# Performance work log

Measured on AMD Instinct MI355X. Metric: run time of the kernel, lower is better.

## Reference

```python
import jax, jax.numpy as jnp
import numpy as np

PLANE_SIZE = 512
N_LEVELS = 8
FEATURE_DIM = 16
N_PTS = 524288


def setup_inputs() -> dict:
    key = jax.random.key(0)
    k1, k2, k3 = jax.random.split(key, 3)
    x = jax.random.uniform(k1, (N_PTS, 3), dtype=jnp.float32)
    # per-point float mip level bias in [0, n_levels-1]
    level = jax.random.uniform(k2, (N_PTS, 1), dtype=jnp.float32) * (N_LEVELS - 1)
    fm = jax.random.uniform(k3, (3, PLANE_SIZE, PLANE_SIZE, FEATURE_DIM),
                            minval=-0.01, maxval=0.01, dtype=jnp.float32)
    return {"x": x, "level": level, "fm": fm, "n_levels": N_LEVELS}


def _bilinear(flat_pyr, offsets, sizes, uv, lvl_i):
    # flat_pyr: (3, T, C) concatenated mip levels; uv: (3, N, 2); lvl_i: (3, N) int32
    size = sizes[lvl_i]                      # (3, N) texture size at this mip
    fsize = size.astype(uv.dtype)
    px = uv[..., 0] * fsize - 0.5            # u -> width axis (nvdiffrast convention)
    py = uv[..., 1] * fsize - 0.5            # v -> height axis
    x0 = jnp.floor(px)
    y0 = jnp.floor(py)
    fx = (px - x0)[..., None]
    fy = (py - y0)[..., None]
    x0i = x0.astype(jnp.int32)
    y0i = y0.astype(jnp.int32)
    xa = jnp.clip(x0i, 0, size - 1)          # boundary_mode='clamp'
    xb = jnp.clip(x0i + 1, 0, size - 1)
    ya = jnp.clip(y0i, 0, size - 1)
    yb = jnp.clip(y0i + 1, 0, size - 1)
    base = offsets[lvl_i]
    p = jnp.arange(3)[:, None]
    g = lambda yy, xx: flat_pyr[p, base + yy * size + xx]   # (3, N, C) gather
    f00 = g(ya, xa); f01 = g(ya, xb); f10 = g(yb, xa); f11 = g(yb, xb)
    return (f00 * (1 - fx) + f01 * fx) * (1 - fy) + (f10 * (1 - fx) + f11 * fx) * fy


def reference(x, level, fm, n_levels):
    N = x.shape[0]
    C = fm.shape[-1]
    # build mip pyramid via 2x2 box filter (nvdiffrast auto-mips)
    levels = [fm]
    for _ in range(n_levels - 1):
        t = levels[-1]
        s = t.shape[1]
        levels.append(t.reshape(3, s // 2, 2, s // 2, 2, C).mean(axis=(2, 4)))
    sizes_list = [l.shape[1] for l in levels]
    offsets = jnp.asarray(np.cumsum([0] + [s * s for s in sizes_list[:-1]]), jnp.int32)
    sizes = jnp.asarray(sizes_list, jnp.int32)
    flat_pyr = jnp.concatenate([l.reshape(3, -1, C) for l in levels], axis=1)  # (3, T, C)
    # tri-plane decomposition: plane0 sees (y,z), plane1 (x,z), plane2 (x,y)
    uv = jnp.stack([x[:, [1, 2]], x[:, [0, 2]], x[:, [0, 1]]], axis=0)  # (3, N, 2)
    max_mip = n_levels - 1
    lvl = jnp.clip(jnp.broadcast_to(level.reshape(1, N), (3, N)), 0.0, float(max_mip))
    l0 = jnp.floor(lvl)
    f = (lvl - l0)[..., None]                # (3, N, 1) level fraction
    l0i = l0.astype(jnp.int32)
    l1i = jnp.minimum(l0i + 1, max_mip)
    s0 = _bilinear(flat_pyr, offsets, sizes, uv, l0i)
    s1 = _bilinear(flat_pyr, offsets, sizes, uv, l1i)
    enc = s0 * (1 - f) + s1 * f              # (3, N, C) trilinear (mip-lerped)
    # permute(1,2,0,3).view(N, 3C): per point, concat plane0|plane1|plane2 features
    return jnp.transpose(enc, (1, 0, 2)).reshape(N, 3 * C)
```

## Files before the change

### kernel.cpp

```cpp
#include <hip/hip_runtime.h>
#include <hip/hip_fp16.h>


typedef float        f4v   __attribute__((ext_vector_type(4)));
typedef unsigned int u32x2 __attribute__((ext_vector_type(2)));
typedef unsigned int u32x4 __attribute__((ext_vector_type(4)));

#define FM_PLANE_STRIDE (262144 * 16)
#define WS_PLANE_STRIDE (87376 * 16)
#define PSTRIDE_H (349520 * 16)
#define WS_H_BYTES (3ull * PSTRIDE_H * 2ull)
#define LVL5_OFF 349184u

__device__ __forceinline__ unsigned lvl_off(int l) {
    return (1048576u - (1048576u >> (2 * l))) / 3u;
}

__device__ __forceinline__ f4v ld4(const float* p) {
    return *reinterpret_cast<const f4v*>(p);
}
__device__ __forceinline__ f4v ld4nt(const float* p) {
    return __builtin_nontemporal_load(reinterpret_cast<const f4v*>(p));
}
__device__ __forceinline__ void st4(float* p, f4v v) {
    *reinterpret_cast<f4v*>(p) = v;
}
__device__ __forceinline__ void st4nt(float* p, f4v v) {
    __builtin_nontemporal_store(v, reinterpret_cast<f4v*>(p));
}
__device__ __forceinline__ f4v ldraw_h(const __half* p) {
    return *reinterpret_cast<const f4v*>(p);
}
__device__ __forceinline__ u32x2 pack4(f4v v) {
    __half2 lo = __floats2half2_rn(v.x, v.y);
    __half2 hi = __floats2half2_rn(v.z, v.w);
    u32x2 r;
    r.x = *reinterpret_cast<unsigned*>(&lo);
    r.y = *reinterpret_cast<unsigned*>(&hi);
    return r;
}
__device__ __forceinline__ f4v h4f(const __half* p) {
    u32x2 u = *reinterpret_cast<const u32x2*>(p);
    unsigned a0 = u.x, a1 = u.y;
    __half2 lo = *reinterpret_cast<__half2*>(&a0);
    __half2 hi = *reinterpret_cast<__half2*>(&a1);
    float2 flo = __half22float2(lo), fhi = __half22float2(hi);
    f4v r; r.x = flo.x; r.y = flo.y; r.z = fhi.x; r.w = fhi.y;
    return r;
}
__device__ __forceinline__ float2 up2(float rawcomp) {
    unsigned u = __float_as_uint(rawcomp);
    __half2 hh = *reinterpret_cast<__half2*>(&u);
    return __half22float2(hh);
}


__global__ __launch_bounds__(256) void mip_convert_l1(
    const float* __restrict__ fm, __half* __restrict__ wsh)
{
    int t = blockIdx.x * 256 + threadIdx.x;
    const int p = blockIdx.y;
    const int q = t & 3, idx = t >> 2;
    const int y = idx >> 8, x = idx & 255;
    const float* sp = fm + (size_t)p * FM_PLANE_STRIDE
                         + ((size_t)(2 * y) * 512 + 2 * x) * 16 + q * 4;
    f4v a = ld4nt(sp);
    f4v b = ld4nt(sp + 16);
    f4v c = ld4nt(sp + 512 * 16);
    f4v d = ld4nt(sp + 512 * 16 + 16);
    __half* L0 = wsh + (size_t)p * PSTRIDE_H;
    size_t o00 = ((size_t)(2 * y) * 512 + 2 * x) * 16 + q * 4;
    *reinterpret_cast<u32x2*>(L0 + o00)                 = pack4(a);
    *reinterpret_cast<u32x2*>(L0 + o00 + 16)            = pack4(b);
    *reinterpret_cast<u32x2*>(L0 + o00 + 512 * 16)      = pack4(c);
    *reinterpret_cast<u32x2*>(L0 + o00 + 512 * 16 + 16) = pack4(d);
    f4v m = (a + b + c + d) * 0.25f;
    __half* L1 = wsh + (size_t)p * PSTRIDE_H + (size_t)262144 * 16;
    *reinterpret_cast<u32x2*>(L1 + ((size_t)y * 256 + x) * 16 + q * 4) = pack4(m);
}

__global__ __launch_bounds__(256) void mip_tail_h(__half* __restrict__ wsh)
{
    const int tile = blockIdx.x;
    const int q    = blockIdx.y;
    const int p    = blockIdx.z;
    const int ty = tile >> 2, tx = tile & 3;
    const int tid = threadIdx.x;

    __shared__ f4v A[32 * 32];
    __shared__ f4v B[16 * 16];

    __half* plane = wsh + (size_t)p * PSTRIDE_H;
    const __half* L1 = plane + (size_t)lvl_off(1) * 16;
    __half* L2 = plane + (size_t)lvl_off(2) * 16;
    __half* L3 = plane + (size_t)lvl_off(3) * 16;
    __half* L4 = plane + (size_t)lvl_off(4) * 16;
    __half* L5 = plane + (size_t)lvl_off(5) * 16;
    __half* L6 = plane + (size_t)lvl_off(6) * 16;
    __half* L7 = plane + (size_t)lvl_off(7) * 16;

    #pragma unroll
    for (int k = 0; k < 4; ++k) {
        int li = tid + k * 256;
        int ly = li >> 5, lx = li & 31;
        int gy = ty * 32 + ly, gx = tx * 32 + lx;
        const __half* sp = L1 + ((size_t)(2 * gy) * 256 + 2 * gx) * 16 + q * 4;
        f4v r = (h4f(sp) + h4f(sp + 16) + h4f(sp + 256 * 16) + h4f(sp + 256 * 16 + 16)) * 0.25f;
        A[li] = r;
        *reinterpret_cast<u32x2*>(L2 + ((size_t)gy * 128 + gx) * 16 + q * 4) = pack4(r);
    }
    __syncthreads();

    {
        int ly = tid >> 4, lx = tid & 15;
        f4v r = (A[(2 * ly) * 32 + 2 * lx]     + A[(2 * ly) * 32 + 2 * lx + 1] +
                 A[(2 * ly + 1) * 32 + 2 * lx] + A[(2 * ly + 1) * 32 + 2 * lx + 1]) * 0.25f;
        B[tid] = r;
        *reinterpret_cast<u32x2*>(L3 + ((size_t)(ty * 16 + ly) * 64 + tx * 16 + lx) * 16 + q * 4) = pack4(r);
    }
    __syncthreads();

    if (tid < 64) {
        int ly = tid >> 3, lx = tid & 7;
        f4v r = (B[(2 * ly) * 16 + 2 * lx]     + B[(2 * ly) * 16 + 2 * lx + 1] +
                 B[(2 * ly + 1) * 16 + 2 * lx] + B[(2 * ly + 1) * 16 + 2 * lx + 1]) * 0.25f;
        A[tid] = r;
        *reinterpret_cast<u32x2*>(L4 + ((size_t)(ty * 8 + ly) * 32 + tx * 8 + lx) * 16 + q * 4) = pack4(r);
    }
    __syncthreads();

    if (tid < 16) {
        int ly = tid >> 2, lx = tid & 3;
        f4v r = (A[(2 * ly) * 8 + 2 * lx]     + A[(2 * ly) * 8 + 2 * lx + 1] +
                 A[(2 * ly + 1) * 8 + 2 * lx] + A[(2 * ly + 1) * 8 + 2 * lx + 1]) * 0.25f;
        B[tid] = r;
        *reinterpret_cast<u32x2*>(L5 + ((size_t)(ty * 4 + ly) * 16 + tx * 4 + lx) * 16 + q * 4) = pack4(r);
    }
    __syncthreads();

    if (tid < 4) {
        int ly = tid >> 1, lx = tid & 1;
        f4v r = (B[(2 * ly) * 4 + 2 * lx]     + B[(2 * ly) * 4 + 2 * lx + 1] +
                 B[(2 * ly + 1) * 4 + 2 * lx] + B[(2 * ly + 1) * 4 + 2 * lx + 1]) * 0.25f;
        A[tid] = r;
        *reinterpret_cast<u32x2*>(L6 + ((size_t)(ty * 2 + ly) * 8 + tx * 2 + lx) * 16 + q * 4) = pack4(r);
    }
    __syncthreads();

    if (tid == 0) {
        f4v r = (A[0] + A[1] + A[2] + A[3]) * 0.25f;
        *reinterpret_cast<u32x2*>(L7 + ((size_t)ty * 4 + tx) * 16 + q * 4) = pack4(r);
    }
}

__device__ __forceinline__ void tap_issue(
    const __half* __restrict__ wsh, const __half* __restrict__ lds_h,
    int p, int l, float u, float v, int h,
    f4v& q00, f4v& q01, f4v& q10, f4v& q11, float& fx, float& fy)
{
    const int sz = 512 >> l;
    const float fsz = (float)sz;
    float px = u * fsz - 0.5f;
    float py = v * fsz - 0.5f;
    float xf = floorf(px), yf = floorf(py);
    fx = px - xf;
    fy = py - yf;
    int xi = (int)xf, yi = (int)yf;
    int xa = min(max(xi, 0), sz - 1);
    int xb = min(xi + 1, sz - 1);
    int ya = min(max(yi, 0), sz - 1);
    int yb = min(yi + 1, sz - 1);
    if (l >= 5) {
        const int sel = (l == 6) ? 256 : ((l == 7) ? 320 : 0);
        const __half* base = lds_h + (size_t)(p * 336 + sel) * 16 + h * 8;
        const __half* r0 = base + (ya * sz) * 16;
        const __half* r1 = base + (yb * sz) * 16;
        q00 = ldraw_h(r0 + xa * 16);
        q01 = ldraw_h(r0 + xb * 16);
        q10 = ldraw_h(r1 + xa * 16);
        q11 = ldraw_h(r1 + xb * 16);
    } else {
        const __half* base = wsh + (size_t)p * PSTRIDE_H + (size_t)lvl_off(l) * 16 + h * 8;
        const __half* r0 = base + (size_t)(ya * sz) * 16;
        const __half* r1 = base + (size_t)(yb * sz) * 16;
        q00 = ldraw_h(r0 + (size_t)xa * 16);
        q01 = ldraw_h(r0 + (size_t)xb * 16);
        q10 = ldraw_h(r1 + (size_t)xa * 16);
        q11 = ldraw_h(r1 + (size_t)xb * 16);
    }
}

__global__ __launch_bounds__(512, 8) void trimip_sample_h(
    const float* __restrict__ xyz, const float* __restrict__ level,
    const __half* __restrict__ wsh, float* __restrict__ out, int N)
{
    __shared__ u32x4 lds[2016];
    for (int uidx = threadIdx.x; uidx < 2016; uidx += 512) {
        int p = uidx / 672;
        int rem = uidx - p * 672;
        lds[uidx] = *reinterpret_cast<const u32x4*>(
            wsh + (size_t)p * PSTRIDE_H + (size_t)LVL5_OFF * 16 + (size_t)rem * 8);
    }
    __syncthreads();
    const __half* lds_h = reinterpret_cast<const __half*>(lds);

    int t = blockIdx.x * 512 + threadIdx.x;
    if (t >= N * 6) return;
    const int h = t & 1;
    const int r = t >> 1;
    const int n = r / 3;
    const int p = r - n * 3;

    const float c0 = xyz[n * 3 + 0];
    const float c1 = xyz[n * 3 + 1];
    const float c2 = xyz[n * 3 + 2];
    const float u = (p == 0) ? c1 : c0;
    const float v = (p == 2) ? c1 : c2;

    float lv = level[n];
    lv = fminf(fmaxf(lv, 0.f), 7.f);
    float lf = floorf(lv);
    float f = lv - lf;
    int l0 = (int)lf;
    int l1 = min(l0 + 1, 7);

    f4v a00, a01, a10, a11, b00, b01, b10, b11;
    float fx0, fy0, fx1, fy1;
    tap_issue(wsh, lds_h, p, l0, u, v, h, a00, a01, a10, a11, fx0, fy0);
    tap_issue(wsh, lds_h, p, l1, u, v, h, b00, b01, b10, b11, fx1, fy1);

    float s0[8], s1[8];
    {
        float gx = 1.f - fx0, gy = 1.f - fy0;
        float w00 = gx * gy, w01 = fx0 * gy, w10 = gx * fy0, w11 = fx0 * fy0;
        #pragma unroll
        for (int i = 0; i < 4; ++i) {
            float2 a = up2(a00[i]), b = up2(a01[i]), c = up2(a10[i]), d = up2(a11[i]);
            s0[2 * i]     = a.x * w00 + b.x * w01 + c.x * w10 + d.x * w11;
            s0[2 * i + 1] = a.y * w00 + b.y * w01 + c.y * w10 + d.y * w11;
        }
    }
    {
        float gx = 1.f - fx1, gy = 1.f - fy1;
        float w00 = gx * gy, w01 = fx1 * gy, w10 = gx * fy1, w11 = fx1 * fy1;
        #pragma unroll
        for (int i = 0; i < 4; ++i) {
            float2 a = up2(b00[i]), b = up2(b01[i]), c = up2(b10[i]), d = up2(b11[i]);
            s1[2 * i]     = a.x * w00 + b.x * w01 + c.x * w10 + d.x * w11;
            s1[2 * i + 1] = a.y * w00 + b.y * w01 + c.y * w10 + d.y * w11;
        }
    }

    float g = 1.f - f;
    f4v oa, ob;
    #pragma unroll
    for (int i = 0; i < 4; ++i) {
        oa[i] = s0[i] * g + s1[i] * f;
        ob[i] = s0[4 + i] * g + s1[4 + i] * f;
    }
    st4nt(out + (size_t)t * 8, oa);
    st4nt(out + (size_t)t * 8 + 4, ob);
}


__device__ __forceinline__ f4v avg4(f4v a, f4v b, f4v c, f4v d) {
    return (a + b + c + d) * 0.25f;
}

__global__ __launch_bounds__(256) void mip_build_f(
    const float* __restrict__ src, float* __restrict__ dst)
{
    int t = blockIdx.x * blockDim.x + threadIdx.x;
    const int p = blockIdx.y;
    const int q = t & 3, idx = t >> 2;
    const int y = idx >> 8, x = idx & 255;
    const float* sp = src + (size_t)p * FM_PLANE_STRIDE
                          + ((size_t)(2 * y) * 512 + 2 * x) * 16 + q * 4;
    f4v r = avg4(ld4(sp), ld4(sp + 16), ld4(sp + 512 * 16), ld4(sp + 512 * 16 + 16));
    st4(dst + (size_t)p * WS_PLANE_STRIDE + ((size_t)y * 256 + x) * 16 + q * 4, r);
}

__global__ __launch_bounds__(256) void mip_tail_f(float* __restrict__ mips)
{
    const int tile = blockIdx.x, q = blockIdx.y, p = blockIdx.z;
    const int ty = tile >> 2, tx = tile & 3;
    const int tid = threadIdx.x;
    __shared__ f4v A[32 * 32];
    __shared__ f4v B[16 * 16];
    float* plane = mips + (size_t)p * WS_PLANE_STRIDE;
    const float* L1 = plane;
    float* L2 = plane + (size_t)65536 * 16;
    float* L3 = plane + (size_t)81920 * 16;
    float* L4 = plane + (size_t)86016 * 16;
    float* L5 = plane + (size_t)87040 * 16;
    float* L6 = plane + (size_t)87296 * 16;
    float* L7 = plane + (size_t)87360 * 16;

    #pragma unroll
    for (int k = 0; k < 4; ++k) {
        int li = tid + k * 256;
        int ly = li >> 5, lx = li & 31;
        int gy = ty * 32 + ly, gx = tx * 32 + lx;
        const float* sp = L1 + ((size_t)(2 * gy) * 256 + 2 * gx) * 16 + q * 4;
        f4v r = avg4(ld4(sp), ld4(sp + 16), ld4(sp + 256 * 16), ld4(sp + 256 * 16 + 16));
        A[li] = r;
        st4(L2 + ((size_t)gy * 128 + gx) * 16 + q * 4, r);
    }
    __syncthreads();
    {
        int ly = tid >> 4, lx = tid & 15;
        f4v r = avg4(A[(2 * ly) * 32 + 2 * lx],     A[(2 * ly) * 32 + 2 * lx + 1],
                     A[(2 * ly + 1) * 32 + 2 * lx], A[(2 * ly + 1) * 32 + 2 * lx + 1]);
        B[tid] = r;
        st4(L3 + ((size_t)(ty * 16 + ly) * 64 + tx * 16 + lx) * 16 + q * 4, r);
    }
    __syncthreads();
    if (tid < 64) {
        int ly = tid >> 3, lx = tid & 7;
        f4v r = avg4(B[(2 * ly) * 16 + 2 * lx],     B[(2 * ly) * 16 + 2 * lx + 1],
                     B[(2 * ly + 1) * 16 + 2 * lx], B[(2 * ly + 1) * 16 + 2 * lx + 1]);
        A[tid] = r;
        st4(L4 + ((size_t)(ty * 8 + ly) * 32 + tx * 8 + lx) * 16 + q * 4, r);
    }
    __syncthreads();
    if (tid < 16) {
        int ly = tid >> 2, lx = tid & 3;
        f4v r = avg4(A[(2 * ly) * 8 + 2 * lx],     A[(2 * ly) * 8 + 2 * lx + 1],
                     A[(2 * ly + 1) * 8 + 2 * lx], A[(2 * ly + 1) * 8 + 2 * lx + 1]);
        B[tid] = r;
        st4(L5 + ((size_t)(ty * 4 + ly) * 16 + tx * 4 + lx) * 16 + q * 4, r);
    }
    __syncthreads();
    if (tid < 4) {
        int ly = tid >> 1, lx = tid & 1;
        f4v r = avg4(B[(2 * ly) * 4 + 2 * lx],     B[(2 * ly) * 4 + 2 * lx + 1],
                     B[(2 * ly + 1) * 4 + 2 * lx], B[(2 * ly + 1) * 4 + 2 * lx + 1]);
        A[tid] = r;
        st4(L6 + ((size_t)(ty * 2 + ly) * 8 + tx * 2 + lx) * 16 + q * 4, r);
    }
    __syncthreads();
    if (tid == 0) {
        f4v r = avg4(A[0], A[1], A[2], A[3]);
        st4(L7 + ((size_t)ty * 4 + tx) * 16 + q * 4, r);
    }
}

__device__ __forceinline__ f4v bilerp_f(
    const float* __restrict__ fm, const float* __restrict__ mips,
    int p, int l, float u, float v, int q)
{
    const int sz = 512 >> l;
    const float fsz = (float)sz;
    float px = u * fsz - 0.5f;
    float py = v * fsz - 0.5f;
    float xf = floorf(px), yf = floorf(py);
    float fx = px - xf, fy = py - yf;
    int xi = (int)xf, yi = (int)yf;
    int xa = min(max(xi, 0), sz - 1);
    int xb = min(xi + 1, sz - 1);
    int ya = min(max(yi, 0), sz - 1);
    int yb = min(yi + 1, sz - 1);
    const float* base;
    if (l == 0) {
        base = fm + (size_t)p * FM_PLANE_STRIDE;
    } else {
        unsigned off = (262144u - ((unsigned)(sz * sz) << 2)) / 3u;
        base = mips + (size_t)p * WS_PLANE_STRIDE + (size_t)off * 16;
    }
    const float* r0 = base + (size_t)(ya * sz) * 16 + q * 4;
    const float* r1 = base + (size_t)(yb * sz) * 16 + q * 4;
    f4v f00 = ld4(r0 + xa * 16);
    f4v f01 = ld4(r0 + xb * 16);
    f4v f10 = ld4(r1 + xa * 16);
    f4v f11 = ld4(r1 + xb * 16);
    float gx = 1.f - fx, gy = 1.f - fy;
    return (f00 * gx + f01 * fx) * gy + (f10 * gx + f11 * fx) * fy;
}

__global__ __launch_bounds__(256) void trimip_sample_f(
    const float* __restrict__ xyz, const float* __restrict__ level,
    const float* __restrict__ fm, const float* __restrict__ mips,
    float* __restrict__ out, int N)
{
    int t = blockIdx.x * blockDim.x + threadIdx.x;
    if (t >= N * 12) return;
    const int q = t & 3;
    const int r = t >> 2;
    const int n = r / 3;
    const int p = r - n * 3;
    const float c0 = xyz[n * 3 + 0];
    const float c1 = xyz[n * 3 + 1];
    const float c2 = xyz[n * 3 + 2];
    const float u = (p == 0) ? c1 : c0;
    const float v = (p == 2) ? c1 : c2;
    float lv = level[n];
    lv = fminf(fmaxf(lv, 0.f), 7.f);
    float lf = floorf(lv);
    float f = lv - lf;
    int l0 = (int)lf;
    int l1 = min(l0 + 1, 7);
    f4v s0 = bilerp_f(fm, mips, p, l0, u, v, q);
    f4v s1 = bilerp_f(fm, mips, p, l1, u, v, q);
    f4v o = s0 * (1.f - f) + s1 * f;
    st4nt(out + (size_t)t * 4, o);
}

extern "C" void kernel_launch(void* const* d_in, const int* in_sizes, int n_in,
                              void* d_out, int out_size, void* d_ws, size_t ws_size,
                              hipStream_t stream) {
    const float* xyz   = (const float*)d_in[0];
    const float* level = (const float*)d_in[1];
    const float* fm    = (const float*)d_in[2];
    float* out = (float*)d_out;
    const int N = in_sizes[1];

    if (ws_size >= WS_H_BYTES) {
        __half* wsh = (__half*)d_ws;
        mip_convert_l1<<<dim3(1024, 3), dim3(256), 0, stream>>>(fm, wsh);
        mip_tail_h<<<dim3(16, 4, 3), dim3(256), 0, stream>>>(wsh);
        const int total = N * 6;
        trimip_sample_h<<<(total + 511) / 512, 512, 0, stream>>>(xyz, level, wsh, out, N);
    } else {
        float* mips = (float*)d_ws;
        mip_build_f<<<dim3(1024, 3), dim3(256), 0, stream>>>(fm, mips);
        mip_tail_f<<<dim3(16, 4, 3), dim3(256), 0, stream>>>(mips);
        const int total = N * 12;
        trimip_sample_f<<<(total + 255) / 256, 256, 0, stream>>>(xyz, level, fm, mips, out, N);
    }
}
```

Baseline: 200.8 us.

## Split sampling grid per plane and stage mip levels 4-7 in LDS

```diff
diff --git a/kernel.cpp b/kernel.cpp
--- a/kernel.cpp
+++ b/kernel.cpp
@@ -10,7 +10,7 @@
 #define WS_PLANE_STRIDE (87376 * 16)
 #define PSTRIDE_H (349520 * 16)
 #define WS_H_BYTES (3ull * PSTRIDE_H * 2ull)
-#define LVL5_OFF 349184u
+#define LVL4_OFF 348160u
 
 __device__ __forceinline__ unsigned lvl_off(int l) {
     return (1048576u - (1048576u >> (2 * l))) / 3u;
@@ -154,8 +154,8 @@
 }
 
 __device__ __forceinline__ void tap_issue(
-    const __half* __restrict__ wsh, const __half* __restrict__ lds_h,
-    int p, int l, float u, float v, int h,
+    const __half* __restrict__ wplane, const __half* __restrict__ lds_h,
+    int l, float u, float v, int h,
     f4v& q00, f4v& q01, f4v& q10, f4v& q11, float& fx, float& fy)
 {
     const int sz = 512 >> l;
@@ -170,9 +170,8 @@
     int xb = min(xi + 1, sz - 1);
     int ya = min(max(yi, 0), sz - 1);
     int yb = min(yi + 1, sz - 1);
-    if (l >= 5) {
-        const int sel = (l == 6) ? 256 : ((l == 7) ? 320 : 0);
-        const __half* base = lds_h + (size_t)(p * 336 + sel) * 16 + h * 8;
+    if (l >= 4) {
+        const __half* base = lds_h + (size_t)(lvl_off(l) - LVL4_OFF) * 16 + h * 8;
         const __half* r0 = base + (ya * sz) * 16;
         const __half* r1 = base + (yb * sz) * 16;
         q00 = ldraw_h(r0 + xa * 16);
@@ -180,7 +179,7 @@
         q10 = ldraw_h(r1 + xa * 16);
         q11 = ldraw_h(r1 + xb * 16);
     } else {
-        const __half* base = wsh + (size_t)p * PSTRIDE_H + (size_t)lvl_off(l) * 16 + h * 8;
+        const __half* base = wplane + (size_t)lvl_off(l) * 16 + h * 8;
         const __half* r0 = base + (size_t)(ya * sz) * 16;
         const __half* r1 = base + (size_t)(yb * sz) * 16;
         q00 = ldraw_h(r0 + (size_t)xa * 16);
@@ -190,26 +189,23 @@
     }
 }
 
-__global__ __launch_bounds__(512, 8) void trimip_sample_h(
+__global__ __launch_bounds__(512) void trimip_sample_h(
     const float* __restrict__ xyz, const float* __restrict__ level,
     const __half* __restrict__ wsh, float* __restrict__ out, int N)
 {
-    __shared__ u32x4 lds[2016];
-    for (int uidx = threadIdx.x; uidx < 2016; uidx += 512) {
-        int p = uidx / 672;
-        int rem = uidx - p * 672;
+    __shared__ u32x4 lds[2720];
+    const int p = blockIdx.y;
+    const __half* wplane = wsh + (size_t)p * PSTRIDE_H;
+    for (int uidx = threadIdx.x; uidx < 2720; uidx += 512) {
         lds[uidx] = *reinterpret_cast<const u32x4*>(
-            wsh + (size_t)p * PSTRIDE_H + (size_t)LVL5_OFF * 16 + (size_t)rem * 8);
+            wplane + (size_t)LVL4_OFF * 16 + (size_t)uidx * 8);
     }
     __syncthreads();
     const __half* lds_h = reinterpret_cast<const __half*>(lds);
 
-    int t = blockIdx.x * 512 + threadIdx.x;
-    if (t >= N * 6) return;
-    const int h = t & 1;
-    const int r = t >> 1;
-    const int n = r / 3;
-    const int p = r - n * 3;
+    const int n = blockIdx.x * 256 + (threadIdx.x >> 1);
+    if (n >= N) return;
+    const int h = threadIdx.x & 1;
 
     const float c0 = xyz[n * 3 + 0];
     const float c1 = xyz[n * 3 + 1];
@@ -226,8 +222,8 @@
 
     f4v a00, a01, a10, a11, b00, b01, b10, b11;
     float fx0, fy0, fx1, fy1;
-    tap_issue(wsh, lds_h, p, l0, u, v, h, a00, a01, a10, a11, fx0, fy0);
-    tap_issue(wsh, lds_h, p, l1, u, v, h, b00, b01, b10, b11, fx1, fy1);
+    tap_issue(wplane, lds_h, l0, u, v, h, a00, a01, a10, a11, fx0, fy0);
+    tap_issue(wplane, lds_h, l1, u, v, h, b00, b01, b10, b11, fx1, fy1);
 
     float s0[8], s1[8];
     {
@@ -258,8 +254,9 @@
         oa[i] = s0[i] * g + s1[i] * f;
         ob[i] = s0[4 + i] * g + s1[4 + i] * f;
     }
-    st4nt(out + (size_t)t * 8, oa);
-    st4nt(out + (size_t)t * 8 + 4, ob);
+    float* op = out + (size_t)((n * 3 + p) * 2 + h) * 8;
+    st4nt(op, oa);
+    st4nt(op + 4, ob);
 }
 
 
@@ -418,8 +415,8 @@
         __half* wsh = (__half*)d_ws;
         mip_convert_l1<<<dim3(1024, 3), dim3(256), 0, stream>>>(fm, wsh);
         mip_tail_h<<<dim3(16, 4, 3), dim3(256), 0, stream>>>(wsh);
-        const int total = N * 6;
-        trimip_sample_h<<<(total + 511) / 512, 512, 0, stream>>>(xyz, level, wsh, out, N);
+        trimip_sample_h<<<dim3((N + 255) / 256, 3), 512, 0, stream>>>(
+            xyz, level, wsh, out, N);
     } else {
         float* mips = (float*)d_ws;
         mip_build_f<<<dim3(1024, 3), dim3(256), 0, stream>>>(fm, mips);
```

After: 197.7 us. No clear change (-1.5%).
